# Performance work log

Hardware: AMD Instinct MI355X
Metric: run time of the kernel (lower is better)

The kernel has to match this reference:

```python
import jax, jax.numpy as jnp
import numpy as np

K, D, B, T = 512, 256, 32, 4096

def setup_inputs() -> dict:
    key = jax.random.key(0)
    k1, k2 = jax.random.split(key)
    z_e_x = jax.random.normal(k1, (B, D, T), dtype=jnp.float32)
    # nn.Embedding weight init uniform(-1/K, 1/K)
    emb_weight = jax.random.uniform(k2, (K, D), dtype=jnp.float32, minval=-1.0 / K, maxval=1.0 / K)
    return {"z_e_x": z_e_x, "emb_weight": emb_weight}

def reference(z_e_x, emb_weight):
    # forward(): permute [B,D,T] -> [B,T,D], nearest-codebook indices
    z = jnp.transpose(z_e_x, (0, 2, 1))  # [B, T, D]
    # squared L2 distances: ||z||^2 - 2 z.W^T + ||W||^2  -> [B, T, K]
    z_sq = jnp.sum(z * z, axis=-1, keepdims=True)           # [B, T, 1]
    w_sq = jnp.sum(emb_weight * emb_weight, axis=-1)        # [K]
    cross = jnp.einsum('btd,kd->btk', z, emb_weight)        # [B, T, K]
    dists = z_sq - 2.0 * cross + w_sq[None, None, :]
    latents = jnp.argmin(dists, axis=-1)                    # [B, T] int
    return latents
```

## Files before the change

### kernel.cpp

```cpp
#include <hip/hip_runtime.h>
#include <math.h>

#define NK 512
#define DD 256
#define NB 32
#define NT 4096

typedef __attribute__((ext_vector_type(8))) _Float16 f16x8;
typedef __attribute__((ext_vector_type(4))) float f32x4;

#define MARGIN 1.5e-4f
#define DCH 16
#define NCH 16
#define ASTR 536

__device__ __forceinline__ unsigned short f16bits(float x) {
    _Float16 h = (_Float16)x;
    unsigned short s;
    __builtin_memcpy(&s, &h, 2);
    return s;
}

__global__ __launch_bounds__(512) void prep_kernel(const float* __restrict__ W,
                                                   unsigned short* __restrict__ Wpp,
                                                   float* __restrict__ wsq,
                                                   int* __restrict__ gcnt) {
    const int bx = blockIdx.x;
    const int k  = threadIdx.x;
    if (bx < NCH) {
        const int d0 = bx * DCH;
        float w[16];
        const float4* src4 = (const float4*)(W + (size_t)k * DD + d0);
        #pragma unroll
        for (int q = 0; q < 4; ++q) {
            float4 v = src4[q];
            w[4 * q + 0] = v.x; w[4 * q + 1] = v.y; w[4 * q + 2] = v.z; w[4 * q + 3] = v.w;
        }
        __align__(16) unsigned int dw[16];
        #pragma unroll
        for (int j = 0; j < 16; ++j) {
            unsigned short s = f16bits(w[j] * 4096.0f);
            dw[j] = (unsigned int)s | ((unsigned int)s << 16);
        }
        unsigned short* dst = Wpp + ((size_t)bx * 512 + k) * 32;
        #pragma unroll
        for (int j = 0; j < 4; ++j) ((int4*)dst)[j] = ((const int4*)dw)[j];
    } else {
        const float4* row = (const float4*)(W + (size_t)k * DD);
        double s = 0.0;
        #pragma unroll 8
        for (int i = 0; i < DD / 4; ++i) {
            float4 v = row[i];
            s += (double)v.x * v.x + (double)v.y * v.y + (double)v.z * v.z + (double)v.w * v.w;
        }
        wsq[k] = (float)s;
        if (k == 0) *gcnt = 0;
    }
}

__global__ __launch_bounds__(256, 2) void vq_phase1(const float* __restrict__ Z,
                                                    const unsigned short* __restrict__ Wpp,
                                                    const float* __restrict__ wsq,
                                                    int* __restrict__ out,
                                                    int* __restrict__ gties,
                                                    int* __restrict__ gcnt) {
    __shared__ __align__(16) short As[64 * ASTR];
    __shared__ int lcnt, gbase;

    const int tid  = threadIdx.x;
    const int wave = tid >> 6;
    const int lane = tid & 63;
    const int lm   = lane & 15;
    const int lq   = lane >> 4;
    const int nw   = wave;

    const int bx = blockIdx.x;
    const int b  = bx >> 6;
    const int t0 = (bx & 63) * 64;

    const int t_l = tid & 63;
    const int dgs = tid >> 6;

    const float* zcol = Z + (size_t)b * DD * NT + t0 + t_l;

    if (tid == 0) lcnt = 0;

    double zacc = 0.0;
    #pragma unroll
    for (int half = 0; half < 2; ++half) {
        float zv[32];
        #pragma unroll
        for (int j = 0; j < 32; ++j)
            zv[j] = zcol[(size_t)(dgs * 64 + half * 32 + j) * NT];
        #pragma unroll
        for (int j = 0; j < 32; ++j)
            zacc = fma((double)zv[j], (double)zv[j], zacc);
        #pragma unroll
        for (int j0 = 0; j0 < 32; j0 += 4) {
            __align__(16) unsigned int u[4];
            #pragma unroll
            for (int q = 0; q < 4; ++q) {
                float z = zv[j0 + q];
                _Float16 zh = (_Float16)z;
                float rz = z - (float)zh;
                unsigned short hs, ls;
                __builtin_memcpy(&hs, &zh, 2);
                ls = f16bits(rz);
                u[q] = (unsigned int)hs | ((unsigned int)ls << 16);
            }
            *(int4*)&As[t_l * ASTR + (dgs * 64 + half * 32 + j0) * 2] = *(const int4*)u;
        }
    }
    __syncthreads();

    const unsigned short* wb = Wpp + ((size_t)(nw * 128 + lm) * 32) + lq * 8;

    f32x4 acc[4][8];
    #pragma unroll
    for (int mt = 0; mt < 4; ++mt)
        #pragma unroll
        for (int nt = 0; nt < 8; ++nt)
            acc[mt][nt] = (f32x4){0.f, 0.f, 0.f, 0.f};

    int4 bv0[8], bv1[8];
    #pragma unroll
    for (int nt = 0; nt < 8; ++nt)
        bv0[nt] = *(const int4*)(wb + nt * 512);

    #pragma unroll
    for (int c = 0; c < NCH; ++c) {
        int4* cur = (c & 1) ? bv1 : bv0;
        int4* nxt = (c & 1) ? bv0 : bv1;
        if (c < NCH - 1) {
            const unsigned short* wp = wb + (size_t)(c + 1) * 16384;
            #pragma unroll
            for (int nt = 0; nt < 8; ++nt)
                nxt[nt] = *(const int4*)(wp + nt * 512);
        }
        f16x8 a[4];
        #pragma unroll
        for (int mt = 0; mt < 4; ++mt)
            a[mt] = *(const f16x8*)&As[(mt * 16 + lm) * ASTR + c * 32 + lq * 8];
        #pragma unroll
        for (int mt = 0; mt < 4; ++mt)
            #pragma unroll
            for (int nt = 0; nt < 8; ++nt)
                acc[mt][nt] = __builtin_amdgcn_mfma_f32_16x16x32_f16(
                    a[mt], *(const f16x8*)&cur[nt], acc[mt][nt], 0, 0, 0);
    }

    __syncthreads();
    double* zred = (double*)As;
    float*  zf   = (float*)(As + 1024);
    float*  cb1  = (float*)(As + 1536);
    float*  cb2  = (float*)(As + 2048);
    int*    cbi  = (int*)(As + 2560);
    int*    llist = (int*)(As + 3072);

    zred[dgs * 64 + t_l] = zacc;
    __syncthreads();
    if (tid < 64) {
        double s = zred[tid];
        #pragma unroll
        for (int p = 1; p < 4; ++p) s += zred[p * 64 + tid];
        zf[tid] = (float)s;
    }
    __syncthreads();

    float wq[8];
    #pragma unroll
    for (int nt = 0; nt < 8; ++nt)
        wq[nt] = wsq[nw * 128 + nt * 16 + lm];
    const int kbase = nw * 128 + lm;

    #pragma unroll
    for (int mt = 0; mt < 4; ++mt) {
        #pragma unroll
        for (int r = 0; r < 4; ++r) {
            float zz = zf[mt * 16 + lq * 4 + r];
            float q1 = INFINITY, q2 = INFINITY;
            int i1 = 0x7fffffff;
            #pragma unroll
            for (int nt = 0; nt < 8; ++nt) {
                float c2   = __fmul_rn(acc[mt][nt][r], 4.8828125e-4f);
                float dist = __fadd_rn(__fsub_rn(zz, c2), wq[nt]);
                int kk = kbase + nt * 16;
                if (dist < q1 || (dist == q1 && kk < i1)) { q2 = q1; q1 = dist; i1 = kk; }
                else if (dist < q2) q2 = dist;
            }
            #pragma unroll
            for (int mk = 1; mk <= 8; mk <<= 1) {
                float o1 = __shfl_xor(q1, mk);
                float o2 = __shfl_xor(q2, mk);
                int   oi = __shfl_xor(i1, mk);
                if (o1 < q1 || (o1 == q1 && oi < i1)) { q2 = fminf(q1, o2); q1 = o1; i1 = oi; }
                else { q2 = fminf(o1, q2); }
            }
            if (lm == 0) {
                int m = mt * 16 + lq * 4 + r;
                cb1[m * 4 + nw] = q1;
                cb2[m * 4 + nw] = q2;
                cbi[m * 4 + nw] = i1;
            }
        }
    }
    __syncthreads();
    if (tid < 64) {
        float q1 = cb1[tid * 4], q2 = cb2[tid * 4];
        int   i1 = cbi[tid * 4];
        #pragma unroll
        for (int p = 1; p < 4; ++p) {
            float c1 = cb1[tid * 4 + p], c2v = cb2[tid * 4 + p];
            int   ci = cbi[tid * 4 + p];
            if (c1 < q1 || (c1 == q1 && ci < i1)) { q2 = fminf(q1, c2v); q1 = c1; i1 = ci; }
            else { q2 = fminf(q2, c1); }
        }
        out[(size_t)b * NT + t0 + tid] = i1;
        if (q2 - q1 <= MARGIN) {
            int p = atomicAdd(&lcnt, 1);
            llist[p] = b * NT + t0 + tid;
        }
    }
    __syncthreads();
    if (tid == 0) gbase = (lcnt > 0) ? atomicAdd(gcnt, lcnt) : 0;
    __syncthreads();
    if (tid < lcnt) gties[gbase + tid] = llist[tid];
}

__global__ __launch_bounds__(256) void vq_fix(const float* __restrict__ Z,
                                              const float* __restrict__ W,
                                              const float* __restrict__ wsq,
                                              const int* __restrict__ gties,
                                              const int* __restrict__ gcnt,
                                              int* __restrict__ out) {
    __shared__ __align__(16) float Zs[8][256];
    __shared__ double pz[8][32];
    __shared__ float  zsqs[8];
    __shared__ int    bts[8];
    __shared__ float  rv[8][4];
    __shared__ int    ri[8][4];

    const int tid  = threadIdx.x;
    const int lane = tid & 63;
    const int wvx  = tid >> 6;
    const int n    = *gcnt;

    for (int base = blockIdx.x * 8; base < n; base += (int)gridDim.x * 8) {
        const int m = (n - base < 8) ? (n - base) : 8;
        __syncthreads();
        if (tid < 8) bts[tid] = gties[base + ((tid < m) ? tid : 0)];
        __syncthreads();

        #pragma unroll
        for (int i = 0; i < 8; ++i) {
            if (i < m) {
                int tb = bts[i];
                int bb = tb >> 12, t = tb & 4095;
                Zs[i][tid] = Z[(size_t)bb * DD * NT + (size_t)tid * NT + t];
            }
        }
        __syncthreads();

        {
            int i = tid >> 5, seg = tid & 31;
            double s = 0.0;
            #pragma unroll
            for (int j = 0; j < 8; ++j) {
                double zz = (double)Zs[i][seg * 8 + j];
                s = fma(zz, zz, s);
            }
            pz[i][seg] = s;
        }
        __syncthreads();
        if (tid < 8) {
            double s = 0.0;
            #pragma unroll
            for (int j = 0; j < 32; ++j) s += pz[tid][j];
            zsqs[tid] = (float)s;
        }
        __syncthreads();

        float da[2][8];
        #pragma unroll
        for (int rr = 0; rr < 2; ++rr) {
            int k = tid + rr * 256;
            const float4* wr = (const float4*)(W + (size_t)k * DD);
            float a8[8];
            #pragma unroll
            for (int i = 0; i < 8; ++i) a8[i] = 0.f;
            #pragma unroll 2
            for (int q = 0; q < 64; ++q) {
                float4 w4 = wr[q];
                #pragma unroll
                for (int i = 0; i < 8; ++i) {
                    float4 z4 = *(const float4*)&Zs[i][4 * q];
                    a8[i] = fmaf(z4.x, w4.x, a8[i]);
                    a8[i] = fmaf(z4.y, w4.y, a8[i]);
                    a8[i] = fmaf(z4.z, w4.z, a8[i]);
                    a8[i] = fmaf(z4.w, w4.w, a8[i]);
                }
            }
            float wqv = wsq[k];
            #pragma unroll
            for (int i = 0; i < 8; ++i)
                da[rr][i] = __fadd_rn(__fsub_rn(zsqs[i], __fmul_rn(2.0f, a8[i])), wqv);
        }

        #pragma unroll
        for (int i = 0; i < 8; ++i) {
            float v = da[0][i]; int ix = tid;
            if (da[1][i] < v) { v = da[1][i]; ix = tid + 256; }
            #pragma unroll
            for (int mk = 1; mk <= 32; mk <<= 1) {
                float ov = __shfl_xor(v, mk);
                int   oi = __shfl_xor(ix, mk);
                if (ov < v || (ov == v && oi < ix)) { v = ov; ix = oi; }
            }
            if (lane == 0) { rv[i][wvx] = v; ri[i][wvx] = ix; }
        }
        __syncthreads();
        if (tid < 8 && tid < m) {
            float v = INFINITY; int ix = 0x7fffffff;
            #pragma unroll
            for (int w = 0; w < 4; ++w) {
                if (rv[tid][w] < v || (rv[tid][w] == v && ri[tid][w] < ix)) {
                    v = rv[tid][w]; ix = ri[tid][w];
                }
            }
            out[bts[tid]] = ix;
        }
    }
}

#define BT 128
#define BK 128
#define DCHUNK 32
#define NKC (NK / BK)
#define NDC (DD / DCHUNK)
#define WSTR (BK + 4)

__global__ __launch_bounds__(256) void vq_fallback(const float* __restrict__ Z,
                                                   const float* __restrict__ W,
                                                   int* __restrict__ out) {
    __shared__ __align__(16) float Zs[DCHUNK * BT];
    __shared__ __align__(16) float Ws[DCHUNK * WSTR];
    __shared__ float wsqs[NK];

    const int tid = threadIdx.x;
    const int tx  = tid & 15;
    const int ty  = tid >> 4;
    const int b   = blockIdx.y;
    const int t0  = blockIdx.x * BT;

    for (int k = tid; k < NK; k += 256) {
        const float4* row = (const float4*)(W + (size_t)k * DD);
        double s = 0.0;
        for (int i = 0; i < DD / 4; ++i) {
            float4 v = row[i];
            s += (double)v.x * v.x + (double)v.y * v.y + (double)v.z * v.z + (double)v.w * v.w;
        }
        wsqs[k] = (float)s;
    }

    const float* Zb = Z + (size_t)b * DD * NT + t0;

    float best[8]; int bidx[8];
    #pragma unroll
    for (int a = 0; a < 8; ++a) { best[a] = INFINITY; bidx[a] = 0x7fffffff; }
    double zsqd[8];
    #pragma unroll
    for (int a = 0; a < 8; ++a) zsqd[a] = 0.0;
    float zsqf[8];

    for (int kc = 0; kc < NKC; ++kc) {
        float acc[8][8];
        #pragma unroll
        for (int a = 0; a < 8; ++a)
            #pragma unroll
            for (int c = 0; c < 8; ++c) acc[a][c] = 0.f;

        for (int dc = 0; dc < NDC; ++dc) {
            const int d0 = dc * DCHUNK;
            __syncthreads();
            #pragma unroll
            for (int i = 0; i < 4; ++i) {
                int f  = tid + i * 256;
                int r  = f >> 5;
                int c4 = f & 31;
                float4 v = *(const float4*)(Zb + (size_t)(d0 + r) * NT + c4 * 4);
                *(float4*)(&Zs[r * BT + c4 * 4]) = v;
            }
            #pragma unroll
            for (int i = 0; i < 4; ++i) {
                int u  = tid + i * 256;
                int k  = u >> 3;
                int rg = u & 7;
                float4 v = *(const float4*)(W + (size_t)(kc * BK + k) * DD + d0 + rg * 4);
                Ws[(rg * 4 + 0) * WSTR + k] = v.x;
                Ws[(rg * 4 + 1) * WSTR + k] = v.y;
                Ws[(rg * 4 + 2) * WSTR + k] = v.z;
                Ws[(rg * 4 + 3) * WSTR + k] = v.w;
            }
            __syncthreads();
            #pragma unroll 4
            for (int d = 0; d < DCHUNK; ++d) {
                float4 z0 = *(const float4*)(&Zs[d * BT + ty * 8]);
                float4 z1 = *(const float4*)(&Zs[d * BT + ty * 8 + 4]);
                float4 w0 = *(const float4*)(&Ws[d * WSTR + tx * 8]);
                float4 w1 = *(const float4*)(&Ws[d * WSTR + tx * 8 + 4]);
                float za[8] = {z0.x, z0.y, z0.z, z0.w, z1.x, z1.y, z1.z, z1.w};
                float wa[8] = {w0.x, w0.y, w0.z, w0.w, w1.x, w1.y, w1.z, w1.w};
                if (kc == 0) {
                    #pragma unroll
                    for (int a = 0; a < 8; ++a)
                        zsqd[a] = fma((double)za[a], (double)za[a], zsqd[a]);
                }
                #pragma unroll
                for (int a = 0; a < 8; ++a)
                    #pragma unroll
                    for (int c = 0; c < 8; ++c)
                        acc[a][c] = fmaf(za[a], wa[c], acc[a][c]);
            }
        }
        if (kc == 0) {
            #pragma unroll
            for (int a = 0; a < 8; ++a) zsqf[a] = (float)zsqd[a];
        }
        #pragma unroll
        for (int c = 0; c < 8; ++c) {
            int   kg = kc * BK + tx * 8 + c;
            float wqv = wsqs[kg];
            #pragma unroll
            for (int a = 0; a < 8; ++a) {
                float c2   = __fmul_rn(2.0f, acc[a][c]);
                float s    = __fsub_rn(zsqf[a], c2);
                float dist = __fadd_rn(s, wqv);
                if (dist < best[a] || (dist == best[a] && kg < bidx[a])) {
                    best[a] = dist; bidx[a] = kg;
                }
            }
        }
    }
    __syncthreads();
    float* redv = Zs;
    int*   redi = (int*)Ws;
    #pragma unroll
    for (int a = 0; a < 8; ++a) {
        int tl2 = ty * 8 + a;
        redv[tl2 * 16 + tx] = best[a];
        redi[tl2 * 16 + tx] = bidx[a];
    }
    __syncthreads();
    if (tid < BT) {
        float bv = INFINITY; int bi = 0x7fffffff;
        #pragma unroll
        for (int j = 0; j < 16; ++j) {
            float v = redv[tid * 16 + j];
            int   i = redi[tid * 16 + j];
            if (v < bv || (v == bv && i < bi)) { bv = v; bi = i; }
        }
        out[(size_t)b * NT + t0 + tid] = bi;
    }
}

extern "C" void kernel_launch(void* const* d_in, const int* in_sizes, int n_in,
                              void* d_out, int out_size, void* d_ws, size_t ws_size,
                              hipStream_t stream) {
    const float* Z = (const float*)d_in[0];
    const float* W = (const float*)d_in[1];
    int* out = (int*)d_out;

    const size_t OFF_WSQ = 0;
    const size_t OFF_CNT = 2048;
    const size_t OFF_WPP = 4096;
    const size_t OFF_TIE = OFF_WPP + 524288;
    const size_t NEED    = OFF_TIE + 524288;

    if (ws_size >= NEED) {
        float* wsq = (float*)((char*)d_ws + OFF_WSQ);
        int*   gcnt = (int*)((char*)d_ws + OFF_CNT);
        unsigned short* wpp = (unsigned short*)((char*)d_ws + OFF_WPP);
        int*   gties = (int*)((char*)d_ws + OFF_TIE);

        prep_kernel<<<dim3(NCH + 1), dim3(512), 0, stream>>>(W, wpp, wsq, gcnt);
        vq_phase1<<<dim3(2048), dim3(256), 0, stream>>>(Z, wpp, wsq, out, gties, gcnt);
        vq_fix<<<dim3(256), dim3(256), 0, stream>>>(Z, W, wsq, gties, gcnt, out);
    } else {
        vq_fallback<<<dim3(NT / BT, NB), dim3(256), 0, stream>>>(Z, W, out);
    }
}
```

Measured before the change: 340.3 us.

## Pre-split Z into swizzled fp16 hi/lo rows and stream via global_load_lds

Adds a prep_z kernel that transposes Z once into a 128MB workspace of swizzled fp16 hi/lo pairs, plus per-row squared norms computed in double. The main kernel then fills LDS with direct global-to-LDS 16-byte loads instead of doing the strided transpose and conversion itself. This pays an extra full pass over Z (read 128MB, write 128MB) in exchange for a simpler, bandwidth-friendly main loop. The path runs only when the workspace is large enough; otherwise the old kernel is used.

```diff
diff --git a/kernel.cpp b/kernel.cpp
--- a/kernel.cpp
+++ b/kernel.cpp
@@ -19,6 +19,12 @@
     unsigned short s;
     __builtin_memcpy(&s, &h, 2);
     return s;
+}
+
+__device__ __forceinline__ void gl_lds16(const void* g, void* l) {
+    __builtin_amdgcn_global_load_lds(
+        (const __attribute__((address_space(1))) unsigned int*)(g),
+        (__attribute__((address_space(3))) unsigned int*)(l), 16, 0, 0);
 }
 
 __global__ __launch_bounds__(512) void prep_kernel(const float* __restrict__ W,
@@ -58,12 +64,215 @@
     }
 }
 
-__global__ __launch_bounds__(256, 2) void vq_phase1(const float* __restrict__ Z,
-                                                    const unsigned short* __restrict__ Wpp,
-                                                    const float* __restrict__ wsq,
-                                                    int* __restrict__ out,
-                                                    int* __restrict__ gties,
-                                                    int* __restrict__ gcnt) {
+__global__ __launch_bounds__(256) void prep_z(const float* __restrict__ Z,
+                                              unsigned short* __restrict__ Zt,
+                                              float* __restrict__ zsq) {
+    const int tid = threadIdx.x;
+    const int bt  = blockIdx.x * 256 + tid;
+    const int bb  = bt >> 12;
+    const int t   = bt & 4095;
+
+    const float* zc = Z + (size_t)bb * DD * NT + t;
+    char* row = (char*)Zt + ((size_t)bt << 10);
+    const int swz = (t & 7) << 4;
+
+    double p[4];
+    #pragma unroll
+    for (int seg = 0; seg < 4; ++seg) {
+        double s = 0.0;
+        #pragma unroll
+        for (int g = 0; g < 8; ++g) {
+            const int d0 = seg * 64 + g * 8;
+            float zv[8];
+            #pragma unroll
+            for (int j = 0; j < 8; ++j)
+                zv[j] = zc[(size_t)(d0 + j) * NT];
+            #pragma unroll
+            for (int j = 0; j < 8; ++j)
+                s = fma((double)zv[j], (double)zv[j], s);
+            __align__(16) unsigned int u[8];
+            #pragma unroll
+            for (int j = 0; j < 8; ++j) {
+                float z = zv[j];
+                _Float16 zh = (_Float16)z;
+                float rz = z - (float)zh;
+                unsigned short hs, ls;
+                __builtin_memcpy(&hs, &zh, 2);
+                ls = f16bits(rz);
+                u[j] = (unsigned int)hs | ((unsigned int)ls << 16);
+            }
+            *(int4*)(row + (((d0 * 4) + 0) ^ swz))  = ((const int4*)u)[0];
+            *(int4*)(row + (((d0 * 4) + 16) ^ swz)) = ((const int4*)u)[1];
+        }
+        p[seg] = s;
+    }
+    zsq[bt] = (float)(((p[0] + p[1]) + p[2]) + p[3]);
+}
+
+__global__ __launch_bounds__(256, 2) void vq_phase1_gl(const unsigned short* __restrict__ Zt,
+                                                       const float* __restrict__ zsqg,
+                                                       const unsigned short* __restrict__ Wpp,
+                                                       const float* __restrict__ wsq,
+                                                       int* __restrict__ out,
+                                                       int* __restrict__ gties,
+                                                       int* __restrict__ gcnt) {
+    __shared__ __align__(16) short As[64 * 512];
+    __shared__ int lcnt, gbase;
+
+    const int tid  = threadIdx.x;
+    const int wave = tid >> 6;
+    const int lane = tid & 63;
+    const int lm   = lane & 15;
+    const int lq   = lane >> 4;
+    const int nw   = wave;
+
+    const int bx  = blockIdx.x;
+    const int bt0 = bx * 64;
+    const int b   = bx >> 6;
+    const int t0  = (bx & 63) * 64;
+
+    if (tid == 0) lcnt = 0;
+
+    {
+        const char* zbase = (const char*)Zt + ((size_t)bt0 << 10);
+        #pragma unroll
+        for (int i = 0; i < 16; ++i) {
+            const int row = wave * 16 + i;
+            gl_lds16(zbase + ((size_t)row << 10) + ((size_t)lane << 4),
+                     &As[row * 512]);
+        }
+    }
+    __syncthreads();
+
+    const unsigned short* wb = Wpp + ((size_t)(nw * 128 + lm) * 32) + lq * 8;
+
+    f32x4 acc[4][8];
+    #pragma unroll
+    for (int mt = 0; mt < 4; ++mt)
+        #pragma unroll
+        for (int nt = 0; nt < 8; ++nt)
+            acc[mt][nt] = (f32x4){0.f, 0.f, 0.f, 0.f};
+
+    int4 bvA[8], bvB[8];
+    #pragma unroll
+    for (int nt = 0; nt < 8; ++nt)
+        bvA[nt] = *(const int4*)(wb + nt * 512);
+
+    #pragma unroll
+    for (int i = 0; i < 8; ++i) {
+        const int cA = 2 * i, cB = 2 * i + 1;
+        {
+            const unsigned short* wp = wb + (size_t)cB * 16384;
+            #pragma unroll
+            for (int nt = 0; nt < 8; ++nt)
+                bvB[nt] = *(const int4*)(wp + nt * 512);
+        }
+        {
+            f16x8 a[4];
+            #pragma unroll
+            for (int mt = 0; mt < 4; ++mt)
+                a[mt] = *(const f16x8*)&As[(mt * 16 + lm) * 512 +
+                                           ((cA * 32 + lq * 8) ^ ((lm & 7) << 3))];
+            #pragma unroll
+            for (int mt = 0; mt < 4; ++mt)
+                #pragma unroll
+                for (int nt = 0; nt < 8; ++nt)
+                    acc[mt][nt] = __builtin_amdgcn_mfma_f32_16x16x32_f16(
+                        a[mt], *(const f16x8*)&bvA[nt], acc[mt][nt], 0, 0, 0);
+        }
+        if (i < 7) {
+            const unsigned short* wp = wb + (size_t)(cB + 1) * 16384;
+            #pragma unroll
+            for (int nt = 0; nt < 8; ++nt)
+                bvA[nt] = *(const int4*)(wp + nt * 512);
+        }
+        {
+            f16x8 a[4];
+            #pragma unroll
+            for (int mt = 0; mt < 4; ++mt)
+                a[mt] = *(const f16x8*)&As[(mt * 16 + lm) * 512 +
+                                           ((cB * 32 + lq * 8) ^ ((lm & 7) << 3))];
+            #pragma unroll
+            for (int mt = 0; mt < 4; ++mt)
+                #pragma unroll
+                for (int nt = 0; nt < 8; ++nt)
+                    acc[mt][nt] = __builtin_amdgcn_mfma_f32_16x16x32_f16(
+                        a[mt], *(const f16x8*)&bvB[nt], acc[mt][nt], 0, 0, 0);
+        }
+    }
+
+    __syncthreads();
+    float* cb1   = (float*)As;
+    float* cb2   = (float*)(As + 512);
+    int*   cbi   = (int*)(As + 1024);
+    int*   llist = (int*)(As + 1536);
+
+    float wq[8];
+    #pragma unroll
+    for (int nt = 0; nt < 8; ++nt)
+        wq[nt] = wsq[nw * 128 + nt * 16 + lm];
+    const int kbase = nw * 128 + lm;
+
+    #pragma unroll
+    for (int mt = 0; mt < 4; ++mt) {
+        #pragma unroll
+        for (int r = 0; r < 4; ++r) {
+            float zz = zsqg[bt0 + mt * 16 + lq * 4 + r];
+            float q1 = INFINITY, q2 = INFINITY;
+            int i1 = 0x7fffffff;
+            #pragma unroll
+            for (int nt = 0; nt < 8; ++nt) {
+                float c2   = __fmul_rn(acc[mt][nt][r], 4.8828125e-4f);
+                float dist = __fadd_rn(__fsub_rn(zz, c2), wq[nt]);
+                int kk = kbase + nt * 16;
+                if (dist < q1 || (dist == q1 && kk < i1)) { q2 = q1; q1 = dist; i1 = kk; }
+                else if (dist < q2) q2 = dist;
+            }
+            #pragma unroll
+            for (int mk = 1; mk <= 8; mk <<= 1) {
+                float o1 = __shfl_xor(q1, mk);
+                float o2 = __shfl_xor(q2, mk);
+                int   oi = __shfl_xor(i1, mk);
+                if (o1 < q1 || (o1 == q1 && oi < i1)) { q2 = fminf(q1, o2); q1 = o1; i1 = oi; }
+                else { q2 = fminf(o1, q2); }
+            }
+            if (lm == 0) {
+                int m = mt * 16 + lq * 4 + r;
+                cb1[m * 4 + nw] = q1;
+                cb2[m * 4 + nw] = q2;
+                cbi[m * 4 + nw] = i1;
+            }
+        }
+    }
+    __syncthreads();
+    if (tid < 64) {
+        float q1 = cb1[tid * 4], q2 = cb2[tid * 4];
+        int   i1 = cbi[tid * 4];
+        #pragma unroll
+        for (int p = 1; p < 4; ++p) {
+            float c1 = cb1[tid * 4 + p], c2v = cb2[tid * 4 + p];
+            int   ci = cbi[tid * 4 + p];
+            if (c1 < q1 || (c1 == q1 && ci < i1)) { q2 = fminf(q1, c2v); q1 = c1; i1 = ci; }
+            else { q2 = fminf(q2, c1); }
+        }
+        out[bt0 + tid] = i1;
+        if (q2 - q1 <= MARGIN) {
+            int p = atomicAdd(&lcnt, 1);
+            llist[p] = bt0 + tid;
+        }
+    }
+    __syncthreads();
+    if (tid == 0) gbase = (lcnt > 0) ? atomicAdd(gcnt, lcnt) : 0;
+    __syncthreads();
+    if (tid < lcnt) gties[gbase + tid] = llist[tid];
+}
+
+__global__ __launch_bounds__(256, 2) void vq_phase1_reg(const float* __restrict__ Z,
+                                                        const unsigned short* __restrict__ Wpp,
+                                                        const float* __restrict__ wsq,
+                                                        int* __restrict__ out,
+                                                        int* __restrict__ gties,
+                                                        int* __restrict__ gcnt) {
     __shared__ __align__(16) short As[64 * ASTR];
     __shared__ int lcnt, gbase;
 
@@ -472,18 +681,38 @@
 
     const size_t OFF_WSQ = 0;
     const size_t OFF_CNT = 2048;
-    const size_t OFF_WPP = 4096;
+    const size_t OFF_ZSQ = 4096;
+    const size_t OFF_WPP = OFF_ZSQ + 524288;
     const size_t OFF_TIE = OFF_WPP + 524288;
-    const size_t NEED    = OFF_TIE + 524288;
-
-    if (ws_size >= NEED) {
-        float* wsq = (float*)((char*)d_ws + OFF_WSQ);
+    const size_t OFF_ZT  = OFF_TIE + 524288;
+    const size_t NEED_BIG = OFF_ZT + 134217728;
+
+    const size_t T2_WSQ = 0;
+    const size_t T2_CNT = 2048;
+    const size_t T2_WPP = 4096;
+    const size_t T2_TIE = T2_WPP + 524288;
+    const size_t NEED_T2 = T2_TIE + 524288;
+
+    if (ws_size >= NEED_BIG) {
+        float* wsq  = (float*)((char*)d_ws + OFF_WSQ);
         int*   gcnt = (int*)((char*)d_ws + OFF_CNT);
+        float* zsq  = (float*)((char*)d_ws + OFF_ZSQ);
         unsigned short* wpp = (unsigned short*)((char*)d_ws + OFF_WPP);
         int*   gties = (int*)((char*)d_ws + OFF_TIE);
+        unsigned short* zt = (unsigned short*)((char*)d_ws + OFF_ZT);
 
         prep_kernel<<<dim3(NCH + 1), dim3(512), 0, stream>>>(W, wpp, wsq, gcnt);
-        vq_phase1<<<dim3(2048), dim3(256), 0, stream>>>(Z, wpp, wsq, out, gties, gcnt);
+        prep_z<<<dim3(512), dim3(256), 0, stream>>>(Z, zt, zsq);
+        vq_phase1_gl<<<dim3(2048), dim3(256), 0, stream>>>(zt, zsq, wpp, wsq, out, gties, gcnt);
+        vq_fix<<<dim3(256), dim3(256), 0, stream>>>(Z, W, wsq, gties, gcnt, out);
+    } else if (ws_size >= NEED_T2) {
+        float* wsq  = (float*)((char*)d_ws + T2_WSQ);
+        int*   gcnt = (int*)((char*)d_ws + T2_CNT);
+        unsigned short* wpp = (unsigned short*)((char*)d_ws + T2_WPP);
+        int*   gties = (int*)((char*)d_ws + T2_TIE);
+
+        prep_kernel<<<dim3(NCH + 1), dim3(512), 0, stream>>>(W, wpp, wsq, gcnt);
+        vq_phase1_reg<<<dim3(2048), dim3(256), 0, stream>>>(Z, wpp, wsq, out, gties, gcnt);
         vq_fix<<<dim3(256), dim3(256), 0, stream>>>(Z, W, wsq, gties, gcnt, out);
     } else {
         vq_fallback<<<dim3(NT / BT, NB), dim3(256), 0, stream>>>(Z, W, out);
```

Result: slower. 486.6 us (+43.0%).
